# Kernel optimization log

Measured on AMD Instinct MI355X. Metric: run time of the kernel, lower is better.

## Reference

```python
import jax, jax.numpy as jnp
import numpy as np

B, S, E, D = 4, 4096, 512, 64

def setup_inputs() -> dict:
    key = jax.random.key(0)
    kx, kq, kk, kv = jax.random.split(key, 4)
    # xavier_normal std = sqrt(2/(E+D))
    std = float(np.sqrt(2.0 / (E + D)))
    return {
        "x": jax.random.normal(kx, (B, S, E), dtype=jnp.float32),
        "WQ": jax.random.normal(kq, (E, D), dtype=jnp.float32) * std,
        "WK": jax.random.normal(kk, (E, D), dtype=jnp.float32) * std,
        "WV": jax.random.normal(kv, (E, D), dtype=jnp.float32) * std,
    }

def reference(x, WQ, WK, WV):
    # Single-head causal attention; NOTE: scale uses embedding_size (E), as in source.
    Q = x @ WQ  # [B,S,D]
    K = x @ WK
    V = x @ WV
    scale = 1.0 / jnp.sqrt(jnp.float32(E))
    scores = jnp.einsum("bqd,bkd->bqk", Q, K) * scale  # [B,S,S]
    s = scores.shape[1]
    causal = jnp.tril(jnp.ones((s, s), dtype=bool))  # True = keep
    scores = jnp.where(causal[None, :, :], scores, -jnp.inf)
    attn = jax.nn.softmax(scores, axis=2)
    return jnp.einsum("bqk,bkd->bqd", attn, V)
```

## Files before the change

kernel.cpp:

```cpp
#include <hip/hip_runtime.h>
#include <hip/hip_bf16.h>

namespace {
constexpr int B = 4, S = 4096, E = 512, D = 64;
constexpr int CHUNK = 8;
constexpr float SCALE_LOG2E = 0.04419417382415922f * 1.4426950408889634f;

typedef __bf16 bf16x8 __attribute__((ext_vector_type(8)));
typedef float floatx4 __attribute__((ext_vector_type(4)));
}

__global__ __launch_bounds__(256) void prep_wt(
    const float* __restrict__ WQ, const float* __restrict__ WK,
    const float* __restrict__ WV, __bf16* __restrict__ Wt)
{
    __shared__ __bf16 tile[64][72];
    const int t = threadIdx.x;
    const int mat = blockIdx.x >> 3;
    const int k0  = (blockIdx.x & 7) * 64;
    const float* W = (mat == 0) ? WQ : (mat == 1) ? WK : WV;
    #pragma unroll
    for (int i = 0; i < 16; ++i) {
        const int k = (t >> 6) + i * 4;
        tile[t & 63][k] = (__bf16)W[(k0 + k) * 64 + (t & 63)];
    }
    __syncthreads();
    #pragma unroll
    for (int i = 0; i < 2; ++i) {
        const int u = t + 256 * i;
        const int n = u >> 3, kseg = (u & 7) * 8;
        *(bf16x8*)(Wt + (mat * 64 + n) * 512 + k0 + kseg) =
            *(const bf16x8*)&tile[n][kseg];
    }
}

__global__ __launch_bounds__(256) void qkv_mfma(
    const float* __restrict__ x, const __bf16* __restrict__ Wt,
    __bf16* __restrict__ Qb, __bf16* __restrict__ Kb, __bf16* __restrict__ Vt)
{
    __shared__ __bf16 xs[32][72];
    __shared__ __bf16 vsh[64][40];

    const int t = threadIdx.x;
    const int wave = t >> 6, lane = t & 63, quad = lane >> 4, l16 = lane & 15;
    const long row0 = (long)blockIdx.x * 32;
    const int xrr = t >> 3, xcc = (t & 7) * 8;

    const __bf16* wbase = Wt + (wave * 48 + l16) * 512 + quad * 8;

    floatx4 acc[2][3];
    #pragma unroll
    for (int m = 0; m < 2; ++m)
        #pragma unroll
        for (int n = 0; n < 3; ++n) acc[m][n] = (floatx4){0.f, 0.f, 0.f, 0.f};

    float4 xf0, xf1;
    bf16x8 wf[6];
    {
        const float* src = x + (row0 + xrr) * E + xcc;
        xf0 = *(const float4*)src;
        xf1 = *(const float4*)(src + 4);
        #pragma unroll
        for (int ns = 0; ns < 3; ++ns)
            #pragma unroll
            for (int ch = 0; ch < 2; ++ch)
                wf[ns * 2 + ch] = *(const bf16x8*)(wbase + ns * 16 * 512 + ch * 32);
    }

    #pragma unroll
    for (int kc = 0; kc < 8; ++kc) {
        __syncthreads();
        {
            bf16x8 v;
            v[0] = (__bf16)xf0.x; v[1] = (__bf16)xf0.y;
            v[2] = (__bf16)xf0.z; v[3] = (__bf16)xf0.w;
            v[4] = (__bf16)xf1.x; v[5] = (__bf16)xf1.y;
            v[6] = (__bf16)xf1.z; v[7] = (__bf16)xf1.w;
            *(bf16x8*)&xs[xrr][xcc] = v;
        }
        __syncthreads();

        bf16x8 wcur[6];
        #pragma unroll
        for (int i = 0; i < 6; ++i) wcur[i] = wf[i];

        if (kc < 7) {
            const float* src = x + (row0 + xrr) * E + (kc + 1) * 64 + xcc;
            xf0 = *(const float4*)src;
            xf1 = *(const float4*)(src + 4);
            #pragma unroll
            for (int ns = 0; ns < 3; ++ns)
                #pragma unroll
                for (int ch = 0; ch < 2; ++ch)
                    wf[ns * 2 + ch] =
                        *(const bf16x8*)(wbase + ns * 16 * 512 + (kc + 1) * 64 + ch * 32);
        }

        bf16x8 aa[2][2];
        #pragma unroll
        for (int m = 0; m < 2; ++m)
            #pragma unroll
            for (int ch = 0; ch < 2; ++ch)
                aa[m][ch] = *(const bf16x8*)&xs[m * 16 + l16][ch * 32 + quad * 8];
        #pragma unroll
        for (int ns = 0; ns < 3; ++ns) {
            #pragma unroll
            for (int ch = 0; ch < 2; ++ch) {
                #pragma unroll
                for (int m = 0; m < 2; ++m)
                    acc[m][ns] = __builtin_amdgcn_mfma_f32_16x16x32_bf16(
                        aa[m][ch], wcur[ns * 2 + ch], acc[m][ns], 0, 0, 0);
            }
        }
    }

    const long bb_ = row0 >> 12;
    const int s0 = (int)(row0 & 4095);
    #pragma unroll
    for (int ns = 0; ns < 3; ++ns) {
        const int g = wave * 3 + ns;
        const int mat = g >> 2;
        const int col = (g & 3) * 16 + l16;
        #pragma unroll
        for (int m = 0; m < 2; ++m) {
            if (mat < 2) {
                __bf16* Out = (mat == 0) ? Qb : Kb;
                #pragma unroll
                for (int r = 0; r < 4; ++r)
                    Out[(row0 + m * 16 + quad * 4 + r) * 64 + col] = (__bf16)acc[m][ns][r];
            } else {
                __bf16 p[4];
                #pragma unroll
                for (int r = 0; r < 4; ++r) p[r] = (__bf16)acc[m][ns][r];
                *(unsigned long long*)&vsh[col][m * 16 + quad * 4] = *(unsigned long long*)p;
            }
        }
    }
    __syncthreads();
    {
        const int d = t >> 2, seg = (t & 3) * 8;
        bf16x8 v = *(const bf16x8*)&vsh[d][seg];
        *(bf16x8*)(Vt + (bb_ * 64 + d) * 4096 + s0 + seg) = v;
    }
}

__global__ __launch_bounds__(256) void attn_kernel(
    const __bf16* __restrict__ Qg, const __bf16* __restrict__ Kg,
    const __bf16* __restrict__ Vt, __bf16* __restrict__ Opart,
    float* __restrict__ Lpart)
{
    __shared__ __bf16 Ks[64][72];
    __shared__ __bf16 Vts[64][72];
    __shared__ __bf16 Ps[4][16][72];

    int g = blockIdx.x;
    int a = 0;
    while (g >= 4 * (a + 1) * (a + 2)) ++a;
    const int rem = g - 4 * a * (a + 1);
    const int qt  = 8 * a + rem / (a + 1);
    const int c   = rem % (a + 1);

    const int b  = blockIdx.y;
    const int q0 = qt * 64;
    const int t  = threadIdx.x;
    const int wave = t >> 6, lane = t & 63, quad = lane >> 4, l16 = lane & 15;

    const int nkt    = qt + 1;
    const int kstart = c * CHUNK;
    const int kend   = min(kstart + CHUNK, nkt);

    const __bf16* qrow = Qg + ((long)(b * S + q0 + wave * 16 + l16)) * D;
    bf16x8 aq[2];
    aq[0] = *(const bf16x8*)(qrow + quad * 8);
    aq[1] = *(const bf16x8*)(qrow + 32 + quad * 8);

    bf16x8 ones;
    #pragma unroll
    for (int j = 0; j < 8; ++j) ones[j] = (__bf16)1.0f;

    floatx4 o[4];
    #pragma unroll
    for (int i = 0; i < 4; ++i) o[i] = (floatx4){0.f, 0.f, 0.f, 0.f};
    floatx4 lsum = (floatx4){0.f, 0.f, 0.f, 0.f};

    const int srow = t >> 2;
    const int sseg = (t & 3) * 16;

    bf16x8 kf0, kf1, vf0, vf1;
    {
        const __bf16* ks = Kg + ((long)(b * S + kstart * 64 + srow)) * D + sseg;
        kf0 = *(const bf16x8*)ks;
        kf1 = *(const bf16x8*)(ks + 8);
        const __bf16* vs = Vt + ((long)(b * 64 + srow)) * 4096 + kstart * 64 + sseg;
        vf0 = *(const bf16x8*)vs;
        vf1 = *(const bf16x8*)(vs + 8);
    }

    for (int ktg = kstart; ktg < kend; ++ktg) {
        const int kbase = ktg * 64;
        __syncthreads();
        *(bf16x8*)&Ks[srow][sseg]      = kf0;
        *(bf16x8*)&Ks[srow][sseg + 8]  = kf1;
        *(bf16x8*)&Vts[srow][sseg]     = vf0;
        *(bf16x8*)&Vts[srow][sseg + 8] = vf1;
        __syncthreads();

        if (ktg + 1 < kend) {
            const __bf16* ks = Kg + ((long)(b * S + kbase + 64 + srow)) * D + sseg;
            kf0 = *(const bf16x8*)ks;
            kf1 = *(const bf16x8*)(ks + 8);
            const __bf16* vs = Vt + ((long)(b * 64 + srow)) * 4096 + kbase + 64 + sseg;
            vf0 = *(const bf16x8*)vs;
            vf1 = *(const bf16x8*)(vs + 8);
        }

        floatx4 sf[4];
        #pragma unroll
        for (int ns = 0; ns < 4; ++ns) {
            floatx4 cacc = (floatx4){0.f, 0.f, 0.f, 0.f};
            #pragma unroll
            for (int ch = 0; ch < 2; ++ch) {
                bf16x8 bk = *(const bf16x8*)&Ks[ns * 16 + l16][ch * 32 + quad * 8];
                cacc = __builtin_amdgcn_mfma_f32_16x16x32_bf16(aq[ch], bk, cacc, 0, 0, 0);
            }
            sf[ns] = cacc;
        }

        if (ktg == nkt - 1) {
            #pragma unroll
            for (int ns = 0; ns < 4; ++ns) {
                const int key = kbase + ns * 16 + l16;
                #pragma unroll
                for (int r = 0; r < 4; ++r) {
                    const int qr = q0 + wave * 16 + quad * 4 + r;
                    if (key > qr) sf[ns][r] = -1e30f;
                }
            }
        }

        #pragma unroll
        for (int ns = 0; ns < 4; ++ns)
            #pragma unroll
            for (int r = 0; r < 4; ++r) {
                float p = __builtin_amdgcn_exp2f(sf[ns][r] * SCALE_LOG2E);
                Ps[wave][quad * 4 + r][ns * 16 + l16] = (__bf16)p;
            }

        bf16x8 ap[2];
        ap[0] = *(const bf16x8*)&Ps[wave][l16][quad * 8];
        ap[1] = *(const bf16x8*)&Ps[wave][l16][32 + quad * 8];

        lsum = __builtin_amdgcn_mfma_f32_16x16x32_bf16(ap[0], ones, lsum, 0, 0, 0);
        lsum = __builtin_amdgcn_mfma_f32_16x16x32_bf16(ap[1], ones, lsum, 0, 0, 0);

        #pragma unroll
        for (int dsb = 0; dsb < 4; ++dsb) {
            floatx4 cacc = o[dsb];
            #pragma unroll
            for (int ch = 0; ch < 2; ++ch) {
                bf16x8 bv = *(const bf16x8*)&Vts[dsb * 16 + l16][ch * 32 + quad * 8];
                cacc = __builtin_amdgcn_mfma_f32_16x16x32_bf16(ap[ch], bv, cacc, 0, 0, 0);
            }
            o[dsb] = cacc;
        }
    }

    const long rbase = (long)c * (B * S) + (long)b * S + q0 + wave * 16;
    #pragma unroll
    for (int dsb = 0; dsb < 4; ++dsb)
        #pragma unroll
        for (int r = 0; r < 4; ++r)
            Opart[(rbase + quad * 4 + r) * 64 + dsb * 16 + l16] = (__bf16)o[dsb][r];
    if (l16 == 0) {
        #pragma unroll
        for (int r = 0; r < 4; ++r)
            Lpart[rbase + quad * 4 + r] = lsum[r];
    }
}

__global__ __launch_bounds__(256) void combine_kernel(
    const __bf16* __restrict__ Opart, const float* __restrict__ Lpart,
    float* __restrict__ Og)
{
    const int idx = blockIdx.x * 256 + threadIdx.x;
    const int row = idx >> 3, seg = (idx & 7) * 8;
    const int qt = (row & (S - 1)) >> 6;
    const int nc = (qt >> 3) + 1;
    float acc[8] = {0, 0, 0, 0, 0, 0, 0, 0};
    float l = 0.f;
    for (int c = 0; c < nc; ++c) {
        bf16x8 ov = *(const bf16x8*)(Opart + ((long)c * (B * S) + row) * 64 + seg);
        l += Lpart[(long)c * (B * S) + row];
        #pragma unroll
        for (int j = 0; j < 8; ++j) acc[j] += (float)ov[j];
    }
    const float invl = 1.f / l;
    float* dst = Og + (long)row * 64 + seg;
    float4 o0 = {acc[0] * invl, acc[1] * invl, acc[2] * invl, acc[3] * invl};
    float4 o1 = {acc[4] * invl, acc[5] * invl, acc[6] * invl, acc[7] * invl};
    *(float4*)dst = o0;
    *(float4*)(dst + 4) = o1;
}

extern "C" void kernel_launch(void* const* d_in, const int* in_sizes, int n_in,
                              void* d_out, int out_size, void* d_ws, size_t ws_size,
                              hipStream_t stream)
{
    const float* x  = (const float*)d_in[0];
    const float* WQ = (const float*)d_in[1];
    const float* WK = (const float*)d_in[2];
    const float* WV = (const float*)d_in[3];
    float* out = (float*)d_out;

    __bf16* Qb = (__bf16*)d_ws;
    __bf16* Kb = Qb + (size_t)B * S * D;
    __bf16* Vt = Kb + (size_t)B * S * D;
    __bf16* Wt = Vt + (size_t)B * S * D;
    __bf16* Opart = Wt + (size_t)3 * E * D;
    float*  Lpart = (float*)(Opart + (size_t)8 * B * S * D);

    prep_wt<<<dim3(24), 256, 0, stream>>>(WQ, WK, WV, Wt);
    qkv_mfma<<<dim3((B * S) / 32), 256, 0, stream>>>(x, Wt, Qb, Kb, Vt);
    attn_kernel<<<dim3(288, B), 256, 0, stream>>>(Qb, Kb, Vt, Opart, Lpart);
    combine_kernel<<<dim3((B * S * 8) / 256), 256, 0, stream>>>(Opart, Lpart, out);
}
```

Measured before the change: 120.3 us.

## Load K/V MFMA fragments directly from global, drop LDS staging and barriers

The attention kernel stops staging K and V tiles through shared memory with two block barriers per tile. Each wave now loads its MFMA operand fragments straight from global memory, relying on cache hits since all four waves read the same tile. It also swaps the MFMA operand order to produce transposed score and output layouts, which allows packed 8-byte stores of P and of the output. The trade-off is that every wave re-reads K and V and the software prefetch of the next tile is gone, so load latency is no longer overlapped.

```diff
diff --git a/kernel.cpp b/kernel.cpp
--- a/kernel.cpp
+++ b/kernel.cpp
@@ -149,8 +149,6 @@
     const __bf16* __restrict__ Vt, __bf16* __restrict__ Opart,
     float* __restrict__ Lpart)
 {
-    __shared__ __bf16 Ks[64][72];
-    __shared__ __bf16 Vts[64][72];
     __shared__ __bf16 Ps[4][16][72];
 
     int g = blockIdx.x;
@@ -183,99 +181,89 @@
     for (int i = 0; i < 4; ++i) o[i] = (floatx4){0.f, 0.f, 0.f, 0.f};
     floatx4 lsum = (floatx4){0.f, 0.f, 0.f, 0.f};
 
-    const int srow = t >> 2;
-    const int sseg = (t & 3) * 16;
-
-    bf16x8 kf0, kf1, vf0, vf1;
-    {
-        const __bf16* ks = Kg + ((long)(b * S + kstart * 64 + srow)) * D + sseg;
-        kf0 = *(const bf16x8*)ks;
-        kf1 = *(const bf16x8*)(ks + 8);
-        const __bf16* vs = Vt + ((long)(b * 64 + srow)) * 4096 + kstart * 64 + sseg;
-        vf0 = *(const bf16x8*)vs;
-        vf1 = *(const bf16x8*)(vs + 8);
-    }
+    const __bf16* Kb_ = Kg + (long)b * S * D;
+    const __bf16* Vb_ = Vt + (long)b * 64 * 4096;
 
     for (int ktg = kstart; ktg < kend; ++ktg) {
         const int kbase = ktg * 64;
-        __syncthreads();
-        *(bf16x8*)&Ks[srow][sseg]      = kf0;
-        *(bf16x8*)&Ks[srow][sseg + 8]  = kf1;
-        *(bf16x8*)&Vts[srow][sseg]     = vf0;
-        *(bf16x8*)&Vts[srow][sseg + 8] = vf1;
-        __syncthreads();
-
-        if (ktg + 1 < kend) {
-            const __bf16* ks = Kg + ((long)(b * S + kbase + 64 + srow)) * D + sseg;
-            kf0 = *(const bf16x8*)ks;
-            kf1 = *(const bf16x8*)(ks + 8);
-            const __bf16* vs = Vt + ((long)(b * 64 + srow)) * 4096 + kbase + 64 + sseg;
-            vf0 = *(const bf16x8*)vs;
-            vf1 = *(const bf16x8*)(vs + 8);
-        }
+
+        bf16x8 kfr[4][2];
+        #pragma unroll
+        for (int ns = 0; ns < 4; ++ns)
+            #pragma unroll
+            for (int ch = 0; ch < 2; ++ch)
+                kfr[ns][ch] = *(const bf16x8*)(
+                    Kb_ + (long)(kbase + ns * 16 + l16) * 64 + ch * 32 + quad * 8);
+
+        bf16x8 vfr[4][2];
+        #pragma unroll
+        for (int dsb = 0; dsb < 4; ++dsb)
+            #pragma unroll
+            for (int ch = 0; ch < 2; ++ch)
+                vfr[dsb][ch] = *(const bf16x8*)(
+                    Vb_ + (long)(dsb * 16 + l16) * 4096 + kbase + ch * 32 + quad * 8);
 
         floatx4 sf[4];
         #pragma unroll
         for (int ns = 0; ns < 4; ++ns) {
             floatx4 cacc = (floatx4){0.f, 0.f, 0.f, 0.f};
             #pragma unroll
-            for (int ch = 0; ch < 2; ++ch) {
-                bf16x8 bk = *(const bf16x8*)&Ks[ns * 16 + l16][ch * 32 + quad * 8];
-                cacc = __builtin_amdgcn_mfma_f32_16x16x32_bf16(aq[ch], bk, cacc, 0, 0, 0);
-            }
+            for (int ch = 0; ch < 2; ++ch)
+                cacc = __builtin_amdgcn_mfma_f32_16x16x32_bf16(
+                    kfr[ns][ch], aq[ch], cacc, 0, 0, 0);
             sf[ns] = cacc;
         }
 
         if (ktg == nkt - 1) {
-            #pragma unroll
-            for (int ns = 0; ns < 4; ++ns) {
-                const int key = kbase + ns * 16 + l16;
+            const int q = q0 + wave * 16 + l16;
+            #pragma unroll
+            for (int ns = 0; ns < 4; ++ns)
                 #pragma unroll
                 for (int r = 0; r < 4; ++r) {
-                    const int qr = q0 + wave * 16 + quad * 4 + r;
-                    if (key > qr) sf[ns][r] = -1e30f;
+                    const int key = kbase + ns * 16 + quad * 4 + r;
+                    if (key > q) sf[ns][r] = -1e30f;
                 }
-            }
-        }
-
-        #pragma unroll
-        for (int ns = 0; ns < 4; ++ns)
-            #pragma unroll
-            for (int r = 0; r < 4; ++r) {
-                float p = __builtin_amdgcn_exp2f(sf[ns][r] * SCALE_LOG2E);
-                Ps[wave][quad * 4 + r][ns * 16 + l16] = (__bf16)p;
-            }
+        }
+
+        #pragma unroll
+        for (int ns = 0; ns < 4; ++ns) {
+            __bf16 p4[4];
+            #pragma unroll
+            for (int r = 0; r < 4; ++r)
+                p4[r] = (__bf16)__builtin_amdgcn_exp2f(sf[ns][r] * SCALE_LOG2E);
+            *(unsigned long long*)&Ps[wave][l16][ns * 16 + quad * 4] =
+                *(unsigned long long*)p4;
+        }
 
         bf16x8 ap[2];
         ap[0] = *(const bf16x8*)&Ps[wave][l16][quad * 8];
         ap[1] = *(const bf16x8*)&Ps[wave][l16][32 + quad * 8];
 
-        lsum = __builtin_amdgcn_mfma_f32_16x16x32_bf16(ap[0], ones, lsum, 0, 0, 0);
-        lsum = __builtin_amdgcn_mfma_f32_16x16x32_bf16(ap[1], ones, lsum, 0, 0, 0);
+        lsum = __builtin_amdgcn_mfma_f32_16x16x32_bf16(ones, ap[0], lsum, 0, 0, 0);
+        lsum = __builtin_amdgcn_mfma_f32_16x16x32_bf16(ones, ap[1], lsum, 0, 0, 0);
 
         #pragma unroll
         for (int dsb = 0; dsb < 4; ++dsb) {
             floatx4 cacc = o[dsb];
             #pragma unroll
-            for (int ch = 0; ch < 2; ++ch) {
-                bf16x8 bv = *(const bf16x8*)&Vts[dsb * 16 + l16][ch * 32 + quad * 8];
-                cacc = __builtin_amdgcn_mfma_f32_16x16x32_bf16(ap[ch], bv, cacc, 0, 0, 0);
-            }
+            for (int ch = 0; ch < 2; ++ch)
+                cacc = __builtin_amdgcn_mfma_f32_16x16x32_bf16(
+                    vfr[dsb][ch], ap[ch], cacc, 0, 0, 0);
             o[dsb] = cacc;
         }
     }
 
     const long rbase = (long)c * (B * S) + (long)b * S + q0 + wave * 16;
     #pragma unroll
-    for (int dsb = 0; dsb < 4; ++dsb)
-        #pragma unroll
-        for (int r = 0; r < 4; ++r)
-            Opart[(rbase + quad * 4 + r) * 64 + dsb * 16 + l16] = (__bf16)o[dsb][r];
-    if (l16 == 0) {
-        #pragma unroll
-        for (int r = 0; r < 4; ++r)
-            Lpart[rbase + quad * 4 + r] = lsum[r];
-    }
+    for (int dsb = 0; dsb < 4; ++dsb) {
+        __bf16 p4[4];
+        #pragma unroll
+        for (int r = 0; r < 4; ++r) p4[r] = (__bf16)o[dsb][r];
+        *(unsigned long long*)(Opart + (rbase + l16) * 64 + dsb * 16 + quad * 4) =
+            *(unsigned long long*)p4;
+    }
+    if (quad == 0)
+        Lpart[rbase + l16] = lsum[0];
 }
 
 __global__ __launch_bounds__(256) void combine_kernel(
```

Result: slower. 177.2 us (+47.3%).
